# Kernel optimization log

Hardware: AMD Instinct MI355X
Metric: run time of the kernel (lower is better)

Reference implementation:

```python
import jax, jax.numpy as jnp
import numpy as np

K = 8
W_CONST = 0.01
EPS = 1e-8


def _normalize(v, eps=1e-8):
    return v / (jnp.linalg.norm(v, axis=-1, keepdims=True) + eps)


def _coarse_normal(x, vertices, vertex_normals):
    # x: (N,3); vertices, vertex_normals: (V,3)
    # brute-force KNN (ascending by squared distance, like cKDTree.query)
    d2_all = jnp.sum((x[:, None, :] - vertices[None, :, :]) ** 2, axis=-1)  # (N,V)
    neg_d2, idx = jax.lax.top_k(-d2_all, K)  # sorted ascending distance
    d2 = -neg_d2                                                    # (N,K)
    v_knn = vertices[idx]                                           # (N,K,3)
    n_knn = vertex_normals[idx]                                     # (N,K,3)
    d2c = jnp.maximum(d2, EPS)
    inv_d2 = 1.0 / d2c                                              # (N,K)
    term_knn = jnp.sum(n_knn * inv_d2[..., None], axis=1)           # (N,3)
    v1 = v_knn[:, 0]                                                # nearest vertex
    d2_v1 = jnp.maximum(jnp.sum((x - v1) ** 2, axis=-1), EPS)       # (N,)
    term_dir = (x - v1) / (W_CONST * d2_v1[:, None])
    W = jnp.sum(inv_d2, axis=1) + 1.0 / W_CONST                     # (N,)
    n_tilde = (term_knn + term_dir) / W[:, None]
    nc = _normalize(n_tilde)
    return nc, v1


def _ray_mesh_first_hit(origins, dirs, tri0, e1, e2):
    # Moller-Trumbore, all points vs all faces. origins/dirs: (N,3); tri0/e1/e2: (F,3)
    pvec = jnp.cross(dirs[:, None, :], e2[None, :, :])              # (N,F,3)
    det = jnp.einsum('fk,nfk->nf', e1, pvec)                        # (N,F)
    ok_det = jnp.abs(det) > EPS
    inv_det = jnp.where(ok_det, 1.0 / jnp.where(ok_det, det, 1.0), 0.0)
    tvec = origins[:, None, :] - tri0[None, :, :]                   # (N,F,3)
    u = jnp.sum(tvec * pvec, axis=-1) * inv_det
    qvec = jnp.cross(tvec, e1[None, :, :])                          # (N,F,3)
    v = jnp.einsum('nk,nfk->nf', dirs, qvec) * inv_det
    t = jnp.einsum('fk,nfk->nf', e2, qvec) * inv_det
    valid = ok_det & (u >= 0.0) & (v >= 0.0) & (u + v <= 1.0) & (t > EPS)
    t_masked = jnp.where(valid, t, jnp.inf)
    t_min = jnp.min(t_masked, axis=1)                               # first hit along ray
    hit = jnp.isfinite(t_min)
    loc = origins + dirs * jnp.where(hit, t_min, 0.0)[:, None]
    return hit, loc


def _project(x, vertices, vertex_normals, faces):
    nc, v1 = _coarse_normal(x, vertices, vertex_normals)
    tri0 = vertices[faces[:, 0]]
    e1 = vertices[faces[:, 1]] - tri0
    e2 = vertices[faces[:, 2]] - tri0
    # primary cast along -nc
    hit1, loc1 = _ray_mesh_first_hit(x, -nc, tri0, e1, e2)
    # fallback cast toward nearest vertex
    dir_fb = _normalize(v1 - x)
    hit2, loc2 = _ray_mesh_first_hit(x, dir_fb, tri0, e1, e2)
    xc = jnp.where(hit1[:, None], loc1, jnp.where(hit2[:, None], loc2, v1))
    s = jnp.sum((x - xc) * nc, axis=-1, keepdims=True)              # (N,1)
    return xc, s, nc


def setup_inputs() -> dict:
    key = jax.random.key(0)
    k1, k2, k3, k4 = jax.random.split(key, 4)
    N, V, F = 2048, 8192, 8192
    x = jax.random.normal(k1, (N, 3), dtype=jnp.float32)
    vertices = jax.random.normal(k2, (V, 3), dtype=jnp.float32)
    vertex_normals = _normalize(jax.random.normal(k3, (V, 3), dtype=jnp.float32))
    faces = jax.random.randint(k4, (F, 3), 0, V, dtype=jnp.int32)
    return {"x": x, "vertices": vertices, "vertex_normals": vertex_normals, "faces": faces}


def reference(x, vertices, vertex_normals, faces):
    # returns (xc:(N,3), s:(N,1), nc:(N,3)) like ProjectionFn.forward
    return _project(x, vertices, vertex_normals, faces)
```

## Files before the change

kernel.cpp:

```cpp
#include <hip/hip_runtime.h>
#include <math.h>

#pragma float_control(precise, on)

#define EPSF 1e-8f
#define TRI_CHUNK 32


__global__ void __launch_bounds__(256) knn_kernel(
    const float* __restrict__ x, const float* __restrict__ verts,
    const float* __restrict__ vnorm, float* __restrict__ ncw,
    float* __restrict__ v1w, float* __restrict__ dfbw,
    unsigned int* __restrict__ tmin, int N, int V) {
#pragma clang fp contract(off)
    int p = blockIdx.x;
    int tid = threadIdx.x;
    int wave = tid >> 6;
    int lane = tid & 63;
    if (p >= N) return;

    if (tid < 2) tmin[2 * p + tid] = 0x7f800000u;

    float xx = x[p * 3 + 0];
    float xy = x[p * 3 + 1];
    float xz = x[p * 3 + 2];

    unsigned long long ka[8], kb[8];
#pragma unroll
    for (int i = 0; i < 8; ++i) { ka[i] = ~0ULL; kb[i] = ~0ULL; }

    for (int va = tid; va < V; va += 512) {
        int vb = va + 256;
        bool hasB = vb < V;

        float avx = verts[va * 3 + 0];
        float avy = verts[va * 3 + 1];
        float avz = verts[va * 3 + 2];
        float bvx = 0.f, bvy = 0.f, bvz = 0.f;
        if (hasB) {
            bvx = verts[vb * 3 + 0];
            bvy = verts[vb * 3 + 1];
            bvz = verts[vb * 3 + 2];
        }

        float dxa = xx - avx, dya = xy - avy, dza = xz - avz;
        float d2a = ((dxa * dxa) + (dya * dya)) + (dza * dza);
        unsigned long long kA =
            (((unsigned long long)__float_as_uint(d2a)) << 32) | (unsigned int)va;
        if (kA < ka[7]) {
            ka[7] = kA;
#pragma unroll
            for (int j = 7; j > 0; --j) {
                if (ka[j] < ka[j - 1]) {
                    unsigned long long t = ka[j];
                    ka[j] = ka[j - 1];
                    ka[j - 1] = t;
                }
            }
        }

        if (hasB) {
            float dxb = xx - bvx, dyb = xy - bvy, dzb = xz - bvz;
            float d2b = ((dxb * dxb) + (dyb * dyb)) + (dzb * dzb);
            unsigned long long kB =
                (((unsigned long long)__float_as_uint(d2b)) << 32) | (unsigned int)vb;
            if (kB < kb[7]) {
                kb[7] = kB;
#pragma unroll
                for (int j = 7; j > 0; --j) {
                    if (kb[j] < kb[j - 1]) {
                        unsigned long long t = kb[j];
                        kb[j] = kb[j - 1];
                        kb[j - 1] = t;
                    }
                }
            }
        }
    }

    unsigned long long wsel[8];
#pragma unroll
    for (int j = 0; j < 8; ++j) {
        unsigned long long c = (ka[0] < kb[0]) ? ka[0] : kb[0];
        unsigned long long m = c;
#pragma unroll
        for (int s = 1; s < 64; s <<= 1) {
            unsigned long long o = __shfl_xor(m, s, 64);
            if (o < m) m = o;
        }
        if (c == m) {
            if (ka[0] == m) {
#pragma unroll
                for (int t = 0; t < 7; ++t) ka[t] = ka[t + 1];
                ka[7] = ~0ULL;
            } else {
#pragma unroll
                for (int t = 0; t < 7; ++t) kb[t] = kb[t + 1];
                kb[7] = ~0ULL;
            }
        }
        wsel[j] = m;
    }

    __shared__ unsigned long long cand[32];
    if (lane == 0) {
#pragma unroll
        for (int j = 0; j < 8; ++j) cand[wave * 8 + j] = wsel[j];
    }
    __syncthreads();
    if (wave != 0) return;

    unsigned long long c0 = (lane < 32) ? cand[lane] : ~0ULL;
    unsigned long long sel[8];
#pragma unroll
    for (int j = 0; j < 8; ++j) {
        unsigned long long m = c0;
#pragma unroll
        for (int s = 1; s < 64; s <<= 1) {
            unsigned long long o = __shfl_xor(m, s, 64);
            if (o < m) m = o;
        }
        if (c0 == m) c0 = ~0ULL;
        sel[j] = m;
    }

    if (lane != 0) return;

    float invk[8];
    float nsx = 0.f, nsy = 0.f, nsz = 0.f;
#pragma unroll
    for (int j = 0; j < 8; ++j) {
        int id = (int)(sel[j] & 0xffffffffu);
        float d2 = __uint_as_float((unsigned int)(sel[j] >> 32));
        float inv = 1.0f / fmaxf(d2, EPSF);
        invk[j] = inv;
        nsx = nsx + vnorm[id * 3 + 0] * inv;
        nsy = nsy + vnorm[id * 3 + 1] * inv;
        nsz = nsz + vnorm[id * 3 + 2] * inv;
    }
    float Wsum = ((invk[0] + invk[1]) + (invk[2] + invk[3])) +
                 ((invk[4] + invk[5]) + (invk[6] + invk[7]));

    int id0 = (int)(sel[0] & 0xffffffffu);
    float v1x = verts[id0 * 3 + 0];
    float v1y = verts[id0 * 3 + 1];
    float v1z = verts[id0 * 3 + 2];

    float dxv = xx - v1x, dyv = xy - v1y, dzv = xz - v1z;
    float d2v1 = fmaxf(((dxv * dxv) + (dyv * dyv)) + (dzv * dzv), EPSF);
    float den = 0.01f * d2v1;
    float tdx = dxv / den, tdy = dyv / den, tdz = dzv / den;

    float W = Wsum + 100.0f;
    float ntx = (nsx + tdx) / W;
    float nty = (nsy + tdy) / W;
    float ntz = (nsz + tdz) / W;
    float nrm = sqrtf(((ntx * ntx) + (nty * nty)) + (ntz * ntz)) + 1e-8f;
    float ncx = ntx / nrm, ncy = nty / nrm, ncz = ntz / nrm;

    float fx = v1x - xx, fy = v1y - xy, fz = v1z - xz;
    float fn = sqrtf(((fx * fx) + (fy * fy)) + (fz * fz)) + 1e-8f;
    fx = fx / fn; fy = fy / fn; fz = fz / fn;

    ncw[p * 3 + 0] = ncx; ncw[p * 3 + 1] = ncy; ncw[p * 3 + 2] = ncz;
    v1w[p * 3 + 0] = v1x; v1w[p * 3 + 1] = v1y; v1w[p * 3 + 2] = v1z;
    dfbw[p * 3 + 0] = fx; dfbw[p * 3 + 1] = fy; dfbw[p * 3 + 2] = fz;
}

__global__ void __launch_bounds__(256, 4) ray_kernel(
    const float* __restrict__ x, const float* __restrict__ ncw,
    const float* __restrict__ dfbw, const float* __restrict__ verts,
    const int* __restrict__ faces,
    unsigned int* __restrict__ tmin, int N, int F) {
#pragma clang fp contract(off)
    const float M = 1e-5f;
    __shared__ __align__(16) float sh[TRI_CHUNK * 12];
    int tid = threadIdx.x;
    int cbase = blockIdx.y * TRI_CHUNK;
    int cnt = min(TRI_CHUNK, F - cbase);

    for (int j = tid; j < cnt; j += 256) {
        int fi = cbase + j;
        int f0 = faces[fi * 3 + 0];
        int f1 = faces[fi * 3 + 1];
        int f2 = faces[fi * 3 + 2];
        float t0x = verts[f0 * 3 + 0], t0y = verts[f0 * 3 + 1], t0z = verts[f0 * 3 + 2];
        float ax = verts[f1 * 3 + 0], ay = verts[f1 * 3 + 1], az = verts[f1 * 3 + 2];
        float bx = verts[f2 * 3 + 0], by = verts[f2 * 3 + 1], bz = verts[f2 * 3 + 2];
        float4* s4 = (float4*)(sh + j * 12);
        s4[0] = make_float4(t0x, t0y, t0z, ax - t0x);
        s4[1] = make_float4(ay - t0y, az - t0z, bx - t0x, by - t0y);
        sh[j * 12 + 8] = bz - t0z;
    }
    __syncthreads();

    int pnt = blockIdx.x * 256 + tid;
    if (pnt >= N) return;

    float ox = x[pnt * 3 + 0];
    float oy = x[pnt * 3 + 1];
    float oz = x[pnt * 3 + 2];
    float dax = -ncw[pnt * 3 + 0], day = -ncw[pnt * 3 + 1], daz = -ncw[pnt * 3 + 2];
    float dbx = dfbw[pnt * 3 + 0], dby = dfbw[pnt * 3 + 1], dbz = dfbw[pnt * 3 + 2];

    const float INF = __uint_as_float(0x7f800000u);
    float tba = INF, tbb = INF;
    for (int j = 0; j < cnt; ++j) {
        const float4 A = *(const float4*)(sh + j * 12);
        const float4 B = *(const float4*)(sh + j * 12 + 4);
        const float e2z = sh[j * 12 + 8];
        float e1x = A.w, e1y = B.x, e1z = B.y;
        float e2x = B.z, e2y = B.w;

        float tvx = ox - A.x;
        float tvy = oy - A.y;
        float tvz = oz - A.z;
        float qx = (tvy * e1z) - (tvz * e1y);
        float qy = (tvz * e1x) - (tvx * e1z);
        float qz = (tvx * e1y) - (tvy * e1x);
        float tq = ((e2x * qx) + (e2y * qy)) + (e2z * qz);

        {
            float px = (day * e2z) - (daz * e2y);
            float py = (daz * e2x) - (dax * e2z);
            float pz = (dax * e2y) - (day * e2x);
            float det = ((e1x * px) + (e1y * py)) + (e1z * pz);
            bool ok = fabsf(det) > EPSF;
            float inv = ok ? (1.0f / det) : 0.0f;
            float u = (((tvx * px) + (tvy * py)) + (tvz * pz)) * inv;
            float v = (((dax * qx) + (day * qy)) + (daz * qz)) * inv;
            float t = tq * inv;
            bool valid = ok && (u >= -M) && (v >= -M) && ((u + v) <= 1.0f + M) && (t > EPSF);
            tba = (valid && t < tba) ? t : tba;
        }
        {
            float px = (dby * e2z) - (dbz * e2y);
            float py = (dbz * e2x) - (dbx * e2z);
            float pz = (dbx * e2y) - (dby * e2x);
            float det = ((e1x * px) + (e1y * py)) + (e1z * pz);
            bool ok = fabsf(det) > EPSF;
            float inv = ok ? (1.0f / det) : 0.0f;
            float u = (((tvx * px) + (tvy * py)) + (tvz * pz)) * inv;
            float v = (((dbx * qx) + (dby * qy)) + (dbz * qz)) * inv;
            float t = tq * inv;
            bool valid = ok && (u >= -M) && (v >= -M) && ((u + v) <= 1.0f + M) && (t > EPSF);
            tbb = (valid && t < tbb) ? t : tbb;
        }
    }
    if (tba < INF) atomicMin(&tmin[2 * pnt + 0], __float_as_uint(tba));
    if (tbb < INF) atomicMin(&tmin[2 * pnt + 1], __float_as_uint(tbb));
}

__global__ void finalize_kernel(const float* __restrict__ x,
                                const float* __restrict__ ncw,
                                const float* __restrict__ v1w,
                                const float* __restrict__ dfbw,
                                const unsigned int* __restrict__ tmin,
                                float* __restrict__ out, int N) {
#pragma clang fp contract(off)
    int p = blockIdx.x * blockDim.x + threadIdx.x;
    if (p >= N) return;
    float t1 = __uint_as_float(tmin[2 * p + 0]);
    float t2 = __uint_as_float(tmin[2 * p + 1]);
    bool h1 = t1 < __uint_as_float(0x7f800000u);
    bool h2 = t2 < __uint_as_float(0x7f800000u);

    float xx = x[p * 3 + 0], xy = x[p * 3 + 1], xz = x[p * 3 + 2];
    float ncx = ncw[p * 3 + 0], ncy = ncw[p * 3 + 1], ncz = ncw[p * 3 + 2];

    float xcx, xcy, xcz;
    if (h1) {
        xcx = xx + ((-ncx) * t1);
        xcy = xy + ((-ncy) * t1);
        xcz = xz + ((-ncz) * t1);
    } else if (h2) {
        xcx = xx + (dfbw[p * 3 + 0] * t2);
        xcy = xy + (dfbw[p * 3 + 1] * t2);
        xcz = xz + (dfbw[p * 3 + 2] * t2);
    } else {
        xcx = v1w[p * 3 + 0]; xcy = v1w[p * 3 + 1]; xcz = v1w[p * 3 + 2];
    }
    float s = (((xx - xcx) * ncx) + ((xy - xcy) * ncy)) + ((xz - xcz) * ncz);

    out[p * 3 + 0] = xcx;
    out[p * 3 + 1] = xcy;
    out[p * 3 + 2] = xcz;
    out[3 * N + p] = s;
    out[4 * N + p * 3 + 0] = ncx;
    out[4 * N + p * 3 + 1] = ncy;
    out[4 * N + p * 3 + 2] = ncz;
}

extern "C" void kernel_launch(void* const* d_in, const int* in_sizes, int n_in,
                              void* d_out, int out_size, void* d_ws, size_t ws_size,
                              hipStream_t stream) {
    const float* x     = (const float*)d_in[0];
    const float* verts = (const float*)d_in[1];
    const float* vnorm = (const float*)d_in[2];
    const int*   faces = (const int*)d_in[3];
    int N = in_sizes[0] / 3;
    int V = in_sizes[1] / 3;
    int F = in_sizes[3] / 3;

    unsigned int* tmin = (unsigned int*)d_ws;
    float* ncw  = (float*)(tmin + 2 * N);
    float* v1w  = ncw + 3 * N;
    float* dfbw = v1w + 3 * N;

    hipLaunchKernelGGL(knn_kernel, dim3(N), dim3(256), 0, stream,
                       x, verts, vnorm, ncw, v1w, dfbw, tmin, N, V);
    int chunks = (F + TRI_CHUNK - 1) / TRI_CHUNK;
    int pblocks = (N + 255) / 256;
    hipLaunchKernelGGL(ray_kernel, dim3(pblocks, chunks), dim3(256), 0, stream,
                       x, ncw, dfbw, verts, faces, tmin, N, F);
    hipLaunchKernelGGL(finalize_kernel, dim3((N + 255) / 256), dim3(256), 0, stream,
                       x, ncw, v1w, dfbw, tmin, (float*)d_out, N);
}
```

Before: 145.4 us.

## Fuse triangle prep into KNN kernel and finalize into per-point ray kernel

Triangle setup (vertex gather and edge vectors) moves into the KNN kernel and is written once to a global workspace buffer. The ray kernel changes to one block per point: threads stride over all faces reading precomputed triangles from global memory, then reduce the hit distances with wave shuffles and shared memory. Finalize runs in the same kernel, which removes the atomicMin pass, the tmin initialisation and one launch. The cost is that triangle data now comes from global/L2 rather than LDS, and the prep only covers all faces when N*256 >= F.

```diff
diff --git a/kernel.cpp b/kernel.cpp
--- a/kernel.cpp
+++ b/kernel.cpp
@@ -4,14 +4,14 @@
 #pragma float_control(precise, on)
 
 #define EPSF 1e-8f
-#define TRI_CHUNK 32
-
-
-__global__ void __launch_bounds__(256) knn_kernel(
+
+
+__global__ void __launch_bounds__(256) knn_prep_kernel(
     const float* __restrict__ x, const float* __restrict__ verts,
-    const float* __restrict__ vnorm, float* __restrict__ ncw,
+    const float* __restrict__ vnorm, const int* __restrict__ faces,
+    float* __restrict__ tri, float* __restrict__ ncw,
     float* __restrict__ v1w, float* __restrict__ dfbw,
-    unsigned int* __restrict__ tmin, int N, int V) {
+    int N, int V, int F) {
 #pragma clang fp contract(off)
     int p = blockIdx.x;
     int tid = threadIdx.x;
@@ -19,7 +19,19 @@
     int lane = tid & 63;
     if (p >= N) return;
 
-    if (tid < 2) tmin[2 * p + tid] = 0x7f800000u;
+    int gt = p * 256 + tid;
+    if (gt < F) {
+        int f0 = faces[gt * 3 + 0];
+        int f1 = faces[gt * 3 + 1];
+        int f2 = faces[gt * 3 + 2];
+        float t0x = verts[f0 * 3 + 0], t0y = verts[f0 * 3 + 1], t0z = verts[f0 * 3 + 2];
+        float ax = verts[f1 * 3 + 0], ay = verts[f1 * 3 + 1], az = verts[f1 * 3 + 2];
+        float bx = verts[f2 * 3 + 0], by = verts[f2 * 3 + 1], bz = verts[f2 * 3 + 2];
+        float4* t4 = (float4*)(tri + gt * 12);
+        t4[0] = make_float4(t0x, t0y, t0z, ax - t0x);
+        t4[1] = make_float4(ay - t0y, az - t0z, bx - t0x, by - t0y);
+        t4[2] = make_float4(bz - t0z, 0.f, 0.f, 0.f);
+    }
 
     float xx = x[p * 3 + 0];
     float xy = x[p * 3 + 1];
@@ -167,54 +179,38 @@
     dfbw[p * 3 + 0] = fx; dfbw[p * 3 + 1] = fy; dfbw[p * 3 + 2] = fz;
 }
 
-__global__ void __launch_bounds__(256, 4) ray_kernel(
-    const float* __restrict__ x, const float* __restrict__ ncw,
-    const float* __restrict__ dfbw, const float* __restrict__ verts,
-    const int* __restrict__ faces,
-    unsigned int* __restrict__ tmin, int N, int F) {
+__global__ void __launch_bounds__(256) ray_fin_kernel(
+    const float* __restrict__ x, const float* __restrict__ tri,
+    const float* __restrict__ ncw, const float* __restrict__ v1w,
+    const float* __restrict__ dfbw, float* __restrict__ out, int N, int F) {
 #pragma clang fp contract(off)
     const float M = 1e-5f;
-    __shared__ __align__(16) float sh[TRI_CHUNK * 12];
+    __shared__ unsigned int red[8];
+    int p = blockIdx.x;
     int tid = threadIdx.x;
-    int cbase = blockIdx.y * TRI_CHUNK;
-    int cnt = min(TRI_CHUNK, F - cbase);
-
-    for (int j = tid; j < cnt; j += 256) {
-        int fi = cbase + j;
-        int f0 = faces[fi * 3 + 0];
-        int f1 = faces[fi * 3 + 1];
-        int f2 = faces[fi * 3 + 2];
-        float t0x = verts[f0 * 3 + 0], t0y = verts[f0 * 3 + 1], t0z = verts[f0 * 3 + 2];
-        float ax = verts[f1 * 3 + 0], ay = verts[f1 * 3 + 1], az = verts[f1 * 3 + 2];
-        float bx = verts[f2 * 3 + 0], by = verts[f2 * 3 + 1], bz = verts[f2 * 3 + 2];
-        float4* s4 = (float4*)(sh + j * 12);
-        s4[0] = make_float4(t0x, t0y, t0z, ax - t0x);
-        s4[1] = make_float4(ay - t0y, az - t0z, bx - t0x, by - t0y);
-        sh[j * 12 + 8] = bz - t0z;
-    }
-    __syncthreads();
-
-    int pnt = blockIdx.x * 256 + tid;
-    if (pnt >= N) return;
-
-    float ox = x[pnt * 3 + 0];
-    float oy = x[pnt * 3 + 1];
-    float oz = x[pnt * 3 + 2];
-    float dax = -ncw[pnt * 3 + 0], day = -ncw[pnt * 3 + 1], daz = -ncw[pnt * 3 + 2];
-    float dbx = dfbw[pnt * 3 + 0], dby = dfbw[pnt * 3 + 1], dbz = dfbw[pnt * 3 + 2];
+    int wave = tid >> 6;
+    int lane = tid & 63;
+    if (p >= N) return;
+
+    float xx = x[p * 3 + 0];
+    float xy = x[p * 3 + 1];
+    float xz = x[p * 3 + 2];
+    float ncx = ncw[p * 3 + 0], ncy = ncw[p * 3 + 1], ncz = ncw[p * 3 + 2];
+    float dbx = dfbw[p * 3 + 0], dby = dfbw[p * 3 + 1], dbz = dfbw[p * 3 + 2];
+    float dax = -ncx, day = -ncy, daz = -ncz;
 
     const float INF = __uint_as_float(0x7f800000u);
     float tba = INF, tbb = INF;
-    for (int j = 0; j < cnt; ++j) {
-        const float4 A = *(const float4*)(sh + j * 12);
-        const float4 B = *(const float4*)(sh + j * 12 + 4);
-        const float e2z = sh[j * 12 + 8];
+    for (int fi = tid; fi < F; fi += 256) {
+        const float4 A = *(const float4*)(tri + fi * 12);
+        const float4 B = *(const float4*)(tri + fi * 12 + 4);
+        const float4 C = *(const float4*)(tri + fi * 12 + 8);
         float e1x = A.w, e1y = B.x, e1z = B.y;
-        float e2x = B.z, e2y = B.w;
-
-        float tvx = ox - A.x;
-        float tvy = oy - A.y;
-        float tvz = oz - A.z;
+        float e2x = B.z, e2y = B.w, e2z = C.x;
+
+        float tvx = xx - A.x;
+        float tvy = xy - A.y;
+        float tvz = xz - A.z;
         float qx = (tvy * e1z) - (tvz * e1y);
         float qy = (tvz * e1x) - (tvx * e1z);
         float qz = (tvx * e1y) - (tvy * e1x);
@@ -247,26 +243,26 @@
             tbb = (valid && t < tbb) ? t : tbb;
         }
     }
-    if (tba < INF) atomicMin(&tmin[2 * pnt + 0], __float_as_uint(tba));
-    if (tbb < INF) atomicMin(&tmin[2 * pnt + 1], __float_as_uint(tbb));
-}
-
-__global__ void finalize_kernel(const float* __restrict__ x,
-                                const float* __restrict__ ncw,
-                                const float* __restrict__ v1w,
-                                const float* __restrict__ dfbw,
-                                const unsigned int* __restrict__ tmin,
-                                float* __restrict__ out, int N) {
-#pragma clang fp contract(off)
-    int p = blockIdx.x * blockDim.x + threadIdx.x;
-    if (p >= N) return;
-    float t1 = __uint_as_float(tmin[2 * p + 0]);
-    float t2 = __uint_as_float(tmin[2 * p + 1]);
-    bool h1 = t1 < __uint_as_float(0x7f800000u);
-    bool h2 = t2 < __uint_as_float(0x7f800000u);
-
-    float xx = x[p * 3 + 0], xy = x[p * 3 + 1], xz = x[p * 3 + 2];
-    float ncx = ncw[p * 3 + 0], ncy = ncw[p * 3 + 1], ncz = ncw[p * 3 + 2];
+
+    unsigned int ma = __float_as_uint(tba);
+    unsigned int mb = __float_as_uint(tbb);
+#pragma unroll
+    for (int s = 1; s < 64; s <<= 1) {
+        unsigned int oa = __shfl_xor(ma, s, 64);
+        if (oa < ma) ma = oa;
+        unsigned int ob = __shfl_xor(mb, s, 64);
+        if (ob < mb) mb = ob;
+    }
+    if (lane == 0) { red[wave * 2 + 0] = ma; red[wave * 2 + 1] = mb; }
+    __syncthreads();
+    if (tid != 0) return;
+
+    unsigned int u1 = min(min(red[0], red[2]), min(red[4], red[6]));
+    unsigned int u2 = min(min(red[1], red[3]), min(red[5], red[7]));
+    float t1 = __uint_as_float(u1);
+    float t2 = __uint_as_float(u2);
+    bool h1 = t1 < INF;
+    bool h2 = t2 < INF;
 
     float xcx, xcy, xcz;
     if (h1) {
@@ -274,9 +270,9 @@
         xcy = xy + ((-ncy) * t1);
         xcz = xz + ((-ncz) * t1);
     } else if (h2) {
-        xcx = xx + (dfbw[p * 3 + 0] * t2);
-        xcy = xy + (dfbw[p * 3 + 1] * t2);
-        xcz = xz + (dfbw[p * 3 + 2] * t2);
+        xcx = xx + (dbx * t2);
+        xcy = xy + (dby * t2);
+        xcz = xz + (dbz * t2);
     } else {
         xcx = v1w[p * 3 + 0]; xcy = v1w[p * 3 + 1]; xcz = v1w[p * 3 + 2];
     }
@@ -302,17 +298,13 @@
     int V = in_sizes[1] / 3;
     int F = in_sizes[3] / 3;
 
-    unsigned int* tmin = (unsigned int*)d_ws;
-    float* ncw  = (float*)(tmin + 2 * N);
+    float* tri  = (float*)d_ws;
+    float* ncw  = tri + (size_t)F * 12;
     float* v1w  = ncw + 3 * N;
     float* dfbw = v1w + 3 * N;
 
-    hipLaunchKernelGGL(knn_kernel, dim3(N), dim3(256), 0, stream,
-                       x, verts, vnorm, ncw, v1w, dfbw, tmin, N, V);
-    int chunks = (F + TRI_CHUNK - 1) / TRI_CHUNK;
-    int pblocks = (N + 255) / 256;
-    hipLaunchKernelGGL(ray_kernel, dim3(pblocks, chunks), dim3(256), 0, stream,
-                       x, ncw, dfbw, verts, faces, tmin, N, F);
-    hipLaunchKernelGGL(finalize_kernel, dim3((N + 255) / 256), dim3(256), 0, stream,
-                       x, ncw, v1w, dfbw, tmin, (float*)d_out, N);
+    hipLaunchKernelGGL(knn_prep_kernel, dim3(N), dim3(256), 0, stream,
+                       x, verts, vnorm, faces, tri, ncw, v1w, dfbw, N, V, F);
+    hipLaunchKernelGGL(ray_fin_kernel, dim3(N), dim3(256), 0, stream,
+                       x, tri, ncw, v1w, dfbw, (float*)d_out, N, F);
 }
```

Result: no change. 147.4 us (+1.4%).
